# Kernel tuning notes

Measured on AMD Instinct MI355X. Metric: run time of the kernel, lower is better.

## Reference

```python
import jax, jax.numpy as jnp
import numpy as np
from jax import lax

KERNEL = 3
SAMPLING_RATE = 100.0
N_GRID = 201  # np.linspace(-1, 1, 201) sub-sample grid


def setup_inputs() -> dict:
    key = jax.random.key(0)
    nb, nc, nx, nt = 32, 3, 64, 4096
    xcorr = jax.random.normal(key, (nb, nc, nx, nt), dtype=jnp.float32)
    return {"xcorr": xcorr, "nlag": nt // 2}


def reference(xcorr, nlag):
    nt = xcorr.shape[-1]
    x = jnp.abs(xcorr)  # vabs=True

    # max_pool2d with (1, kernel=3), stride 1, padding (0, 1) -> SAME max over lag axis
    smax = lax.reduce_window(
        x, -jnp.inf, lax.max,
        window_dimensions=(1, 1, 1, KERNEL),
        window_strides=(1, 1, 1, 1),
        padding=[(0, 0), (0, 0), (0, 0), (KERNEL // 2, KERNEL // 2)],
    )
    keep = (smax == x).astype(x.dtype)

    # top-2 local maxima along lag axis (sorted descending, like torch.topk)
    topk_score, topk_idx = lax.top_k(x * keep, 2)
    s0 = topk_score[..., 0]
    s1 = topk_score[..., 1]
    weight = (0.1 + 3.0 * (s0 - s1)) * s0 ** 2
    i0 = topk_idx[..., 0]  # [nb, nc, nx]

    # --- sub-sample interpolation: 3-point spline == parabola through neighbors ---
    offsets = jnp.array([-1, 0, 1], dtype=i0.dtype)
    nbr_idx = jnp.clip(i0[..., None] + offsets, 0, nt - 1)      # [nb,nc,nx,3]
    y = jnp.take_along_axis(x, nbr_idx, axis=-1)                 # [nb,nc,nx,3]
    ym1, y0, yp1 = y[..., 0], y[..., 1], y[..., 2]
    a = 0.5 * (ym1 + yp1) - y0   # quadratic coeff
    b = 0.5 * (yp1 - ym1)        # linear coeff
    c = y0                       # constant

    xg = jnp.linspace(-1.0, 1.0, N_GRID, dtype=x.dtype)          # [201]
    yg = (a[..., None] * xg + b[..., None]) * xg + c[..., None]  # [nb,nc,nx,201]
    ii = jnp.argmax(yg, axis=-1)                                  # [nb,nc,nx]
    sub_shift = xg[ii]
    topk_idx_f = i0.astype(x.dtype) + sub_shift
    topk_score0 = jnp.take_along_axis(yg, ii[..., None], axis=-1)[..., 0]

    # pick the channel with the largest weight
    idx = jnp.argmax(weight, axis=1, keepdims=True)               # [nb,1,nx]
    max_cc = jnp.take_along_axis(topk_score0, idx, axis=1)
    w = jnp.take_along_axis(weight, idx, axis=1)
    shift_idx = jnp.take_along_axis(topk_idx_f, idx, axis=1) - jnp.asarray(nlag, x.dtype)
    shift_t = shift_idx / SAMPLING_RATE

    # stacked: [cc_max, cc_weight, cc_dt, cc_shift], each [nb,1,nx]
    return jnp.stack([max_cc, w, shift_t, shift_idx], axis=0)
```

## Files before the change

### kernel.cpp

```cpp
#include <hip/hip_runtime.h>
#include <math.h>

#define NB 32
#define NC 3
#define NX 64
#define NT 4096
#define NROWS (NB * NC * NX)

struct Quad { float4 a, b, c, d; };

__device__ __forceinline__ Quad load_chunk16(const float* __restrict__ xr,
                                             int coff, int lane) {
    const float* base = xr + (size_t)coff + (size_t)(lane << 4);
    Quad q;
    q.a = *reinterpret_cast<const float4*>(base);
    q.b = *reinterpret_cast<const float4*>(base + 4);
    q.c = *reinterpret_cast<const float4*>(base + 8);
    q.d = *reinterpret_cast<const float4*>(base + 12);
    return q;
}

__device__ __forceinline__ float keep3(float l, float x, float r) {
    const float m = fmaxf(fmaxf(l, x), r);
    return (x == m) ? x : 0.0f;
}

__device__ __forceinline__ void ins(float c, int t, float& m0, int& i0, float& m1) {
    const bool g = c > m0;
    m1 = g ? m0 : fmaxf(m1, c);
    m0 = fmaxf(m0, c);
    i0 = g ? t : i0;
}

__device__ __forceinline__ void scan_chunk16(Quad q, float lmE, float rmE,
                                             int coff, int lane,
                                             float& m0, int& i0, float& m1)
{
    const int tb = coff + (lane << 4);

    const float e0  = fabsf(q.a.x), e1  = fabsf(q.a.y), e2  = fabsf(q.a.z), e3  = fabsf(q.a.w);
    const float e4  = fabsf(q.b.x), e5  = fabsf(q.b.y), e6  = fabsf(q.b.z), e7  = fabsf(q.b.w);
    const float e8  = fabsf(q.c.x), e9  = fabsf(q.c.y), e10 = fabsf(q.c.z), e11 = fabsf(q.c.w);
    const float e12 = fabsf(q.d.x), e13 = fabsf(q.d.y), e14 = fabsf(q.d.z), e15 = fabsf(q.d.w);

    float lm = __shfl_up(e15, 1);
    lm = (lane == 0) ? lmE : lm;
    float rm = __shfl_down(e0, 1);
    rm = (lane == 63) ? rmE : rm;

    ins(keep3(lm,  e0,  e1 ), tb + 0,  m0, i0, m1);
    ins(keep3(e0,  e1,  e2 ), tb + 1,  m0, i0, m1);
    ins(keep3(e1,  e2,  e3 ), tb + 2,  m0, i0, m1);
    ins(keep3(e2,  e3,  e4 ), tb + 3,  m0, i0, m1);
    ins(keep3(e3,  e4,  e5 ), tb + 4,  m0, i0, m1);
    ins(keep3(e4,  e5,  e6 ), tb + 5,  m0, i0, m1);
    ins(keep3(e5,  e6,  e7 ), tb + 6,  m0, i0, m1);
    ins(keep3(e6,  e7,  e8 ), tb + 7,  m0, i0, m1);
    ins(keep3(e7,  e8,  e9 ), tb + 8,  m0, i0, m1);
    ins(keep3(e8,  e9,  e10), tb + 9,  m0, i0, m1);
    ins(keep3(e9,  e10, e11), tb + 10, m0, i0, m1);
    ins(keep3(e10, e11, e12), tb + 11, m0, i0, m1);
    ins(keep3(e11, e12, e13), tb + 12, m0, i0, m1);
    ins(keep3(e12, e13, e14), tb + 13, m0, i0, m1);
    ins(keep3(e13, e14, e15), tb + 14, m0, i0, m1);
    ins(keep3(e14, e15, rm ), tb + 15, m0, i0, m1);
}

__device__ __forceinline__ void merge_acc(float& m0, int& i0, float& m1,
                                          float bm0, int bi0, float bm1)
{
    const bool big = bm0 > m0;
    const float loser = big ? m0 : bm0;
    m1 = fmaxf(fmaxf(m1, bm1), loser);
    m0 = big ? bm0 : m0;
    i0 = big ? bi0 : i0;
}

__global__ __launch_bounds__(256) void scan_rows_kernel(
    const float* __restrict__ xcorr,
    float* __restrict__ wsv0, int* __restrict__ wsi0, float* __restrict__ wsv1)
{
    const int tid  = threadIdx.x;
    const int lane = tid & 63;
    const int wid  = tid >> 6;
    const int row  = blockIdx.x * 4 + wid;

    const float* __restrict__ xr = xcorr + (size_t)row * NT;

    float m0a = -1.0f, m1a = -1.0f; int i0a = 0;
    float m0b = -1.0f, m1b = -1.0f; int i0b = 0;
    float m0c = -1.0f, m1c = -1.0f; int i0c = 0;
    float m0d = -1.0f, m1d = -1.0f; int i0d = 0;

    Quad q0 = load_chunk16(xr, 0,    lane);
    Quad q1 = load_chunk16(xr, 1024, lane);

    Quad q2 = load_chunk16(xr, 2048, lane);
    float nf = __shfl(fabsf(q1.a.x), 0);
    scan_chunk16(q0, -INFINITY, nf, 0, lane, m0a, i0a, m1a);
    float pl = __shfl(fabsf(q0.d.w), 63);

    Quad q3 = load_chunk16(xr, 3072, lane);
    nf = __shfl(fabsf(q2.a.x), 0);
    scan_chunk16(q1, pl, nf, 1024, lane, m0b, i0b, m1b);
    pl = __shfl(fabsf(q1.d.w), 63);

    nf = __shfl(fabsf(q3.a.x), 0);
    scan_chunk16(q2, pl, nf, 2048, lane, m0c, i0c, m1c);
    pl = __shfl(fabsf(q2.d.w), 63);

    scan_chunk16(q3, pl, -INFINITY, 3072, lane, m0d, i0d, m1d);

    merge_acc(m0a, i0a, m1a, m0b, i0b, m1b);
    merge_acc(m0c, i0c, m1c, m0d, i0d, m1d);
    merge_acc(m0a, i0a, m1a, m0c, i0c, m1c);
    float v0 = m0a, v1 = m1a; int i0 = i0a;

    #pragma unroll
    for (int off = 1; off < 64; off <<= 1) {
        const float ov0 = __shfl_xor(v0, off);
        const int   oi0 = __shfl_xor(i0, off);
        const float ov1 = __shfl_xor(v1, off);
        const bool big = (ov0 > v0) || (ov0 == v0 && oi0 < i0);
        const float loser = big ? v0 : ov0;
        v1 = fmaxf(fmaxf(v1, ov1), loser);
        v0 = big ? ov0 : v0;
        i0 = big ? oi0 : i0;
    }

    if (lane == 0) {
        wsv0[row] = v0;
        wsi0[row] = i0;
        wsv1[row] = v1;
    }
}

__global__ __launch_bounds__(256) void epilogue_kernel(
    const float* __restrict__ xcorr,
    const float* __restrict__ wsv0, const int* __restrict__ wsi0,
    const float* __restrict__ wsv1,
    const int*   __restrict__ nlag_p,
    float* __restrict__ out)
{
    const int g = blockIdx.x * 256 + threadIdx.x;
    if (g >= NB * NX) return;
    const int b = g >> 6;
    const int x = g & 63;

    const int r0 = (b * NC + 0) * NX + x;
    const int r1 = (b * NC + 1) * NX + x;
    const int r2 = (b * NC + 2) * NX + x;

    const float m00 = wsv0[r0], m10 = wsv1[r0]; const int p0 = wsi0[r0];
    const float m01 = wsv0[r1], m11 = wsv1[r1]; const int p1 = wsi0[r1];
    const float m02 = wsv0[r2], m12 = wsv1[r2]; const int p2 = wsi0[r2];

    const float w0 = (0.1f + 3.0f * (m00 - m10)) * (m00 * m00);
    const float w1 = (0.1f + 3.0f * (m01 - m11)) * (m01 * m01);
    const float w2 = (0.1f + 3.0f * (m02 - m12)) * (m02 * m02);

    const bool t1 = w1 > w0;
    float bw = t1 ? w1 : w0;
    float bs = t1 ? m01 : m00;
    int   bp = t1 ? p1 : p0;
    int   rs = t1 ? r1 : r0;
    const bool t2 = w2 > bw;
    bw = t2 ? w2 : bw;
    bs = t2 ? m02 : bs;
    bp = t2 ? p2 : bp;
    rs = t2 ? r2 : rs;

    const float* __restrict__ xrs = xcorr + (size_t)rs * NT;

    const float ym1 = fabsf(xrs[bp > 0 ? bp - 1 : 0]);
    const float yp1 = fabsf(xrs[bp < NT - 1 ? bp + 1 : NT - 1]);
    const float A = 0.5f * (ym1 + yp1) - bs;
    const float B = 0.5f * (yp1 - ym1);
    const float C = bs;

    int gi; float bv;
    if (A == 0.0f) {
        gi = (B > 0.0f) ? 200 : 0;
        const float xg = 0.01f * (float)(gi - 100);
        bv = (A * xg + B) * xg + C;
    } else {
        float gv = (1.0f - 0.5f * B / A) * 100.0f;
        gv = fminf(fmaxf(gv, 0.0f), 200.0f);
        const int glo = (int)gv;
        bv = -INFINITY; gi = 0;
        #pragma unroll
        for (int d = -1; d <= 2; ++d) {
            int gg = glo + d;
            gg = gg < 0 ? 0 : (gg > 200 ? 200 : gg);
            const float xg = 0.01f * (float)(gg - 100);
            const float yg = (A * xg + B) * xg + C;
            if (yg > bv) { bv = yg; gi = gg; }
        }
    }

    const float fidx = (float)bp + 0.01f * (float)(gi - 100);
    const float nlagf = (float)(*nlag_p);
    const float shift_idx = fidx - nlagf;
    const int n = NB * NX;
    out[0 * n + g] = bv;
    out[1 * n + g] = bw;
    out[2 * n + g] = shift_idx / 100.0f;
    out[3 * n + g] = shift_idx;
}

extern "C" void kernel_launch(void* const* d_in, const int* in_sizes, int n_in,
                              void* d_out, int out_size, void* d_ws, size_t ws_size,
                              hipStream_t stream) {
    const float* xcorr  = (const float*)d_in[0];
    const int*   nlag_p = (const int*)d_in[1];
    float* out = (float*)d_out;

    float* ws   = (float*)d_ws;
    float* wsv0 = ws;
    int*   wsi0 = (int*)(ws + NROWS);
    float* wsv1 = ws + 2 * NROWS;

    scan_rows_kernel<<<NROWS / 4, 256, 0, stream>>>(xcorr, wsv0, wsi0, wsv1);

    epilogue_kernel<<<(NB * NX + 255) / 256, 256, 0, stream>>>(
        xcorr, wsv0, wsi0, wsv1, nlag_p, out);
}
```

Before: 24.76 us.

## Fuse row scan and channel-select epilogue into one kernel

Merges the per-row top-2 scan and the epilogue into a single kernel. Each block of 192 threads handles one (batch, x) position, with one wave per channel. The three per-channel results go through shared memory, and wave 0 then does the weight selection and parabolic refinement. This removes the second launch and the workspace round trip, at the cost of smaller 3-wave blocks and an idle tail in the epilogue section.

```diff
diff --git a/kernel.cpp b/kernel.cpp
--- a/kernel.cpp
+++ b/kernel.cpp
@@ -5,7 +5,6 @@
 #define NC 3
 #define NX 64
 #define NT 4096
-#define NROWS (NB * NC * NX)
 
 struct Quad { float4 a, b, c, d; };
 
@@ -76,15 +75,22 @@
     i0 = big ? bi0 : i0;
 }
 
-__global__ __launch_bounds__(256) void scan_rows_kernel(
+__global__ __launch_bounds__(192) void detect_peaks_kernel(
     const float* __restrict__ xcorr,
-    float* __restrict__ wsv0, int* __restrict__ wsi0, float* __restrict__ wsv1)
+    const int*   __restrict__ nlag_p,
+    float* __restrict__ out)
 {
+    __shared__ float sv0[NC], sv1[NC];
+    __shared__ int   si0[NC];
+
+    const int g    = blockIdx.x;
+    const int b    = g >> 6;
+    const int x    = g & 63;
     const int tid  = threadIdx.x;
     const int lane = tid & 63;
     const int wid  = tid >> 6;
-    const int row  = blockIdx.x * 4 + wid;
-
+
+    const int row = (b * NC + wid) * NX + x;
     const float* __restrict__ xr = xcorr + (size_t)row * NT;
 
     float m0a = -1.0f, m1a = -1.0f; int i0a = 0;
@@ -128,84 +134,68 @@
         i0 = big ? oi0 : i0;
     }
 
-    if (lane == 0) {
-        wsv0[row] = v0;
-        wsi0[row] = i0;
-        wsv1[row] = v1;
-    }
-}
-
-__global__ __launch_bounds__(256) void epilogue_kernel(
-    const float* __restrict__ xcorr,
-    const float* __restrict__ wsv0, const int* __restrict__ wsi0,
-    const float* __restrict__ wsv1,
-    const int*   __restrict__ nlag_p,
-    float* __restrict__ out)
-{
-    const int g = blockIdx.x * 256 + threadIdx.x;
-    if (g >= NB * NX) return;
-    const int b = g >> 6;
-    const int x = g & 63;
-
-    const int r0 = (b * NC + 0) * NX + x;
-    const int r1 = (b * NC + 1) * NX + x;
-    const int r2 = (b * NC + 2) * NX + x;
-
-    const float m00 = wsv0[r0], m10 = wsv1[r0]; const int p0 = wsi0[r0];
-    const float m01 = wsv0[r1], m11 = wsv1[r1]; const int p1 = wsi0[r1];
-    const float m02 = wsv0[r2], m12 = wsv1[r2]; const int p2 = wsi0[r2];
-
-    const float w0 = (0.1f + 3.0f * (m00 - m10)) * (m00 * m00);
-    const float w1 = (0.1f + 3.0f * (m01 - m11)) * (m01 * m01);
-    const float w2 = (0.1f + 3.0f * (m02 - m12)) * (m02 * m02);
-
-    const bool t1 = w1 > w0;
-    float bw = t1 ? w1 : w0;
-    float bs = t1 ? m01 : m00;
-    int   bp = t1 ? p1 : p0;
-    int   rs = t1 ? r1 : r0;
-    const bool t2 = w2 > bw;
-    bw = t2 ? w2 : bw;
-    bs = t2 ? m02 : bs;
-    bp = t2 ? p2 : bp;
-    rs = t2 ? r2 : rs;
-
-    const float* __restrict__ xrs = xcorr + (size_t)rs * NT;
-
-    const float ym1 = fabsf(xrs[bp > 0 ? bp - 1 : 0]);
-    const float yp1 = fabsf(xrs[bp < NT - 1 ? bp + 1 : NT - 1]);
-    const float A = 0.5f * (ym1 + yp1) - bs;
-    const float B = 0.5f * (yp1 - ym1);
-    const float C = bs;
-
-    int gi; float bv;
-    if (A == 0.0f) {
-        gi = (B > 0.0f) ? 200 : 0;
-        const float xg = 0.01f * (float)(gi - 100);
-        bv = (A * xg + B) * xg + C;
-    } else {
-        float gv = (1.0f - 0.5f * B / A) * 100.0f;
-        gv = fminf(fmaxf(gv, 0.0f), 200.0f);
-        const int glo = (int)gv;
-        bv = -INFINITY; gi = 0;
-        #pragma unroll
-        for (int d = -1; d <= 2; ++d) {
-            int gg = glo + d;
-            gg = gg < 0 ? 0 : (gg > 200 ? 200 : gg);
-            const float xg = 0.01f * (float)(gg - 100);
-            const float yg = (A * xg + B) * xg + C;
-            if (yg > bv) { bv = yg; gi = gg; }
+    if (lane == 0) { sv0[wid] = v0; si0[wid] = i0; sv1[wid] = v1; }
+    __syncthreads();
+
+    if (wid == 0) {
+        const float m00 = sv0[0], m10 = sv1[0]; const int p0 = si0[0];
+        const float m01 = sv0[1], m11 = sv1[1]; const int p1 = si0[1];
+        const float m02 = sv0[2], m12 = sv1[2]; const int p2 = si0[2];
+
+        const float w0 = (0.1f + 3.0f * (m00 - m10)) * (m00 * m00);
+        const float w1 = (0.1f + 3.0f * (m01 - m11)) * (m01 * m01);
+        const float w2 = (0.1f + 3.0f * (m02 - m12)) * (m02 * m02);
+
+        const bool t1 = w1 > w0;
+        float bw = t1 ? w1 : w0;
+        float bs = t1 ? m01 : m00;
+        int   bp = t1 ? p1 : p0;
+        int   cs = t1 ? 1 : 0;
+        const bool t2 = w2 > bw;
+        bw = t2 ? w2 : bw;
+        bs = t2 ? m02 : bs;
+        bp = t2 ? p2 : bp;
+        cs = t2 ? 2 : cs;
+
+        const float* __restrict__ xrs = xcorr + (size_t)((b * NC + cs) * NX + x) * NT;
+
+        const float ym1 = fabsf(xrs[bp > 0 ? bp - 1 : 0]);
+        const float yp1 = fabsf(xrs[bp < NT - 1 ? bp + 1 : NT - 1]);
+        const float A = 0.5f * (ym1 + yp1) - bs;
+        const float B = 0.5f * (yp1 - ym1);
+        const float C = bs;
+
+        int gi; float bv;
+        if (A == 0.0f) {
+            gi = (B > 0.0f) ? 200 : 0;
+            const float xg = 0.01f * (float)(gi - 100);
+            bv = (A * xg + B) * xg + C;
+        } else {
+            float gv = (1.0f - 0.5f * B / A) * 100.0f;
+            gv = fminf(fmaxf(gv, 0.0f), 200.0f);
+            const int glo = (int)gv;
+            bv = -INFINITY; gi = 0;
+            #pragma unroll
+            for (int d = -1; d <= 2; ++d) {
+                int gg = glo + d;
+                gg = gg < 0 ? 0 : (gg > 200 ? 200 : gg);
+                const float xg = 0.01f * (float)(gg - 100);
+                const float yg = (A * xg + B) * xg + C;
+                if (yg > bv) { bv = yg; gi = gg; }
+            }
+        }
+
+        if (lane == 0) {
+            const float fidx = (float)bp + 0.01f * (float)(gi - 100);
+            const float nlagf = (float)(*nlag_p);
+            const float shift_idx = fidx - nlagf;
+            const int n = NB * NX;
+            out[0 * n + g] = bv;
+            out[1 * n + g] = bw;
+            out[2 * n + g] = shift_idx / 100.0f;
+            out[3 * n + g] = shift_idx;
         }
     }
-
-    const float fidx = (float)bp + 0.01f * (float)(gi - 100);
-    const float nlagf = (float)(*nlag_p);
-    const float shift_idx = fidx - nlagf;
-    const int n = NB * NX;
-    out[0 * n + g] = bv;
-    out[1 * n + g] = bw;
-    out[2 * n + g] = shift_idx / 100.0f;
-    out[3 * n + g] = shift_idx;
 }
 
 extern "C" void kernel_launch(void* const* d_in, const int* in_sizes, int n_in,
@@ -215,13 +205,5 @@
     const int*   nlag_p = (const int*)d_in[1];
     float* out = (float*)d_out;
 
-    float* ws   = (float*)d_ws;
-    float* wsv0 = ws;
-    int*   wsi0 = (int*)(ws + NROWS);
-    float* wsv1 = ws + 2 * NROWS;
-
-    scan_rows_kernel<<<NROWS / 4, 256, 0, stream>>>(xcorr, wsv0, wsi0, wsv1);
-
-    epilogue_kernel<<<(NB * NX + 255) / 256, 256, 0, stream>>>(
-        xcorr, wsv0, wsi0, wsv1, nlag_p, out);
-}
+    detect_peaks_kernel<<<NB * NX, 192, 0, stream>>>(xcorr, nlag_p, out);
+}
```

Result: faster. 23.86 us (median of 2 runs) (-3.6%).
